# Kernel optimization log

Hardware: AMD Instinct MI355X
Metric: run time of the kernel (lower is better)

## Reference

```python
import jax, jax.numpy as jnp
import numpy as np
from jax import lax

DN = ('NCHW', 'OIHW', 'NCHW')  # torch conv layout
QMIN, QMAX = -128.0, 127.0     # qint8 range


def setup_inputs() -> dict:
    key = jax.random.key(0)
    k1, k2, k3, k4 = jax.random.split(key, 4)
    B, Cin, Cout, H, W, K = 8, 320, 320, 64, 64, 3
    x = jax.random.normal(k1, (B, Cin, H, W), dtype=jnp.float32)
    # int8 weight values stored as int32 (int_repr of per-channel quantized weight)
    weight_int = jax.random.randint(k2, (Cout, Cin, K, K), -128, 128, dtype=jnp.int32)
    weight_scales = jax.random.uniform(k3, (Cout,), jnp.float32, 0.001, 0.01)
    act_scales = jnp.float32(0.04)        # per-tensor activation scale
    act_zero_points = jnp.float32(3.0)    # per-tensor activation zero point
    act_scales_inv = 1.0 / act_scales
    bias = jax.random.normal(k4, (Cout,), dtype=jnp.float32) * 0.1
    # precomputed buffers (from_float): padding>0 path
    weight_sum_by_input_channels = weight_int.astype(jnp.float32).sum(axis=1, keepdims=True)  # [O,1,K,K]
    scale = weight_scales * act_scales  # fused dequant scale per output channel
    return {
        'x': x,
        'weight_int': weight_int,
        'weight_sum_by_input_channels': weight_sum_by_input_channels,
        'scale': scale,
        'act_scales_inv': act_scales_inv,
        'act_zero_points': act_zero_points,
        'bias': bias,
    }


def reference(x, weight_int, weight_sum_by_input_channels, scale,
              act_scales_inv, act_zero_points, bias):
    stride, pad = 1, 1
    # per-tensor activation quantization: x_int = clamp(round(x/s) + zp)
    x_int = jnp.clip(jnp.round(x * act_scales_inv) + act_zero_points, QMIN, QMAX)
    w = weight_int.astype(jnp.float32)
    # integer conv (emulated in f32): conv(x_int, W_int)
    acc = lax.conv_general_dilated(x_int, w, (stride, stride),
                                   [(pad, pad), (pad, pad)], dimension_numbers=DN)
    # zero-point correction: zp * conv(ones, sum_i W_int) (spatially varying near padding)
    ones = jnp.ones_like(x[:, :1])  # [B,1,H,W]
    corr = lax.conv_general_dilated(ones, weight_sum_by_input_channels, (stride, stride),
                                    [(pad, pad), (pad, pad)], dimension_numbers=DN)
    corr = corr * act_zero_points
    # dequant: per-output-channel scale = w_scale * a_scale, plus float bias
    out = scale[None, :, None, None] * (acc - corr) + bias[None, :, None, None]
    return out
```

## Files before the change

kernel.cpp:

```cpp
#include <hip/hip_runtime.h>
#include <hip/hip_bf16.h>


typedef int v4i __attribute__((ext_vector_type(4)));

typedef const unsigned int __attribute__((address_space(1)))* gas_uptr;
typedef unsigned int __attribute__((address_space(3)))* las_uptr;

#define B_   8
#define CIN  320
#define COUT 320
#define H_   64
#define W_   64
#define HW_  4096
#define HP   66
#define WP   66
#define XPAD_BYTES (B_*HP*WP*CIN)
#define W8_BYTES (COUT*9*CIN)

__global__ __launch_bounds__(256) void repack_bias_kernel(const int* __restrict__ wint,
                                                          unsigned char* __restrict__ w8,
                                                          const float* __restrict__ wsum,
                                                          const float* __restrict__ scale,
                                                          const float* __restrict__ bias,
                                                          const float* __restrict__ zp_p,
                                                          float* __restrict__ be) {
    int j = blockIdx.x * 256 + threadIdx.x;
    if (j < COUT) {
        float s = 0.f;
        #pragma unroll
        for (int tp = 0; tp < 9; ++tp) s += wsum[j*9 + tp];
        be[j] = bias[j] - scale[j] * zp_p[0] * s;
    }
    int co  = j / 720;
    int r   = j - co * 720;
    int tap = r / 80;
    int d   = r - tap * 80;
    int ci  = d * 4;
    const int* base = wint + (co * CIN + ci) * 9 + tap;
    unsigned b0 = (unsigned)(base[0]  & 0xFF);
    unsigned b1 = (unsigned)(base[9]  & 0xFF);
    unsigned b2 = (unsigned)(base[18] & 0xFF);
    unsigned b3 = (unsigned)(base[27] & 0xFF);
    unsigned dword = b0 | (b1 << 8) | (b2 << 16) | (b3 << 24);

    int coT   = co >> 4;
    int colc  = co & 15;
    int chunk = ci >> 6;
    int q     = (ci >> 4) & 3;
    int dw    = (ci >> 2) & 3;
    int lane  = q * 16 + colc;
    int idx   = (((coT * 9 + tap) * 5 + chunk) * 64 + lane) * 4 + dw;
    ((unsigned*)w8)[idx] = dword;
}

__global__ __launch_bounds__(256) void quant_pad_kernel(const float* __restrict__ x,
                                                        unsigned char* __restrict__ xpad,
                                                        const float* __restrict__ inv_p,
                                                        const float* __restrict__ zp_p) {
    __shared__ __align__(16) unsigned lds[64 * 81];
    int bid = blockIdx.x;
    int b  = bid / HP;
    int ph = bid - b * HP;
    int t  = threadIdx.x;
    float inv = inv_p[0];
    float zp  = zp_p[0];
    int zpi = (int)rintf(zp);
    unsigned zd = ((unsigned)(zpi & 0xFF)) * 0x01010101u;

    unsigned* rowbase = (unsigned*)(xpad + (size_t)((b * HP + ph) * WP) * CIN);

    if (ph == 0 || ph == HP - 1) {
        for (int j = t; j < WP * CIN / 4; j += 256) rowbase[j] = zd;
        return;
    }
    int h = ph - 1;
    const float* xrow = x + (size_t)b * CIN * H_ * W_ + h * W_;
    int wq = t & 15;
    int cg = t >> 4;
    #pragma unroll
    for (int i = 0; i < 5; ++i) {
        int ci0 = i * 64 + cg * 4;
        float4 f[4];
        #pragma unroll
        for (int jj = 0; jj < 4; ++jj)
            f[jj] = *(const float4*)(xrow + (size_t)(ci0 + jj) * HW_ + wq * 4);
        #pragma unroll
        for (int k = 0; k < 4; ++k) {
            unsigned d = 0;
            #pragma unroll
            for (int jj = 0; jj < 4; ++jj) {
                float v = (&f[jj].x)[k];
                float q = rintf(v * inv) + zp;
                q = fminf(fmaxf(q, -128.0f), 127.0f);
                int qi = (int)q;
                d |= ((unsigned)(qi & 0xFF)) << (8 * jj);
            }
            lds[(wq * 4 + k) * 81 + (ci0 >> 2)] = d;
        }
    }
    __syncthreads();
    if (t < 80)            rowbase[t] = zd;
    else if (t < 160)      rowbase[65 * 80 + (t - 80)] = zd;
    for (int j = t; j < 64 * 80; j += 256) {
        int p = j / 80;
        int d = j - p * 80;
        rowbase[80 + j] = lds[p * 81 + d];
    }
}

#define CHUNK_SLOTS 1584
#define ROUNDS 7
#define BUF_BYTES (ROUNDS * 256 * 16)

#define CHUNK_BODY(c_, LAST_)                                                   \
{                                                                               \
    const int c__ = (c_);                                                       \
    const unsigned char* ab = Al + (c__ & 1) * BUF_BYTES;                       \
          \
    _Pragma("unroll")                                                           \
    for (int k = 0; k < 3; ++k)                                                 \
        _Pragma("unroll")                                                       \
        for (int mi = 0; mi < 4; ++mi)                                          \
            aB[k][mi] = *(const v4i*)(ab + wm * 4224 + aoffs[k][mi]);           \
    _Pragma("unroll")                                                           \
    for (int tp = 0; tp < 9; ++tp) {                                            \
        const int bank = tp % 3;                                                \
        if (!LAST_ && tp == 0) {     \
            unsigned char* dst = Al + ((c__ + 1) & 1) * BUF_BYTES;              \
            int cio = (c__ + 1) * 64;                                           \
            _Pragma("unroll")                                                   \
            for (int r = 0; r < ROUNDS; ++r)                                    \
                __builtin_amdgcn_global_load_lds(                               \
                    (gas_uptr)(const void*)(xpad + srcoff[r] + cio),            \
                    (las_uptr)(dst + r * 4096 + t * 16), 16, 0, 0);             \
        }                                                                       \
                       \
        __builtin_amdgcn_s_setprio(1);                                          \
        _Pragma("unroll")                                                       \
        for (int mi = 0; mi < 4; ++mi)                                          \
            _Pragma("unroll")                                                   \
            for (int ni = 0; ni < 5; ++ni)                                      \
                acc[mi][ni] = __builtin_amdgcn_mfma_i32_16x16x64_i8(            \
                    aB[bank][mi], bB[bank][ni], acc[mi][ni], 0, 0, 0);          \
        __builtin_amdgcn_s_setprio(0);                                          \
           \
           \
        if (tp < 6) {                                                           \
            _Pragma("unroll")                                                   \
            for (int ni = 0; ni < 5; ++ni)                                      \
                bB[bank][ni] = *(const v4i*)(bbase[ni] + ((tp + 3) * 5 + c__) * 1024);\
            int tn  = tp + 3;                                                   \
            int kh2 = tn / 3;                                                   \
            int kw2 = tn - kh2 * 3;                                             \
            _Pragma("unroll")                                                   \
            for (int mi = 0; mi < 4; ++mi)                                      \
                aB[bank][mi] = *(const v4i*)(ab + (wm + kh2) * 4224 + aoffs[kw2][mi]);\
        } else if (!LAST_) {                                                    \
            _Pragma("unroll")                                                   \
            for (int ni = 0; ni < 5; ++ni)                                      \
                bB[bank][ni] = *(const v4i*)(bbase[ni] + ((tp - 6) * 5 + (c__ + 1)) * 1024);\
        }                                                                       \
    }                                                                           \
}

__global__ __launch_bounds__(256, 2) void conv_gemm_kernel(const unsigned char* __restrict__ xpad,
                                                           const unsigned char* __restrict__ w8,
                                                           const float* __restrict__ scale,
                                                           const float* __restrict__ be,
                                                           float* __restrict__ out) {
    __shared__ __align__(16) unsigned char Al[2 * BUF_BYTES];

    int t    = threadIdx.x;
    int lane = t & 63;
    int wave = t >> 6;
    int wm   = wave;
    int m0   = blockIdx.x * 256;
    int n0   = blockIdx.y * 80;
    int b0   = m0 >> 12;
    int h0   = (m0 & 4095) >> 6;

    int srcoff[ROUNDS];
    #pragma unroll
    for (int r = 0; r < ROUNDS; ++r) {
        int slot = r * 256 + t;
        if (slot >= CHUNK_SLOTS) slot = 0;
        int R   = slot / 264;
        int rem = slot - R * 264;
        int C   = rem >> 2;
        int ql  = rem & 3;
        int qs  = ql ^ ((C >> 1) & 3);
        srcoff[r] = ((b0 * HP + h0 + R) * WP + C) * CIN + qs * 16;
    }

    int colc = lane & 15;
    int q    = lane >> 4;

    int aoffs[3][4];
    #pragma unroll
    for (int kw = 0; kw < 3; ++kw)
        #pragma unroll
        for (int mi = 0; mi < 4; ++mi) {
            int C = mi * 16 + colc + kw;
            aoffs[kw][mi] = C * 64 + ((q ^ ((C >> 1) & 3)) * 16);
        }

    const unsigned char* bbase[5];
    int coT0 = n0 >> 4;
    #pragma unroll
    for (int ni = 0; ni < 5; ++ni)
        bbase[ni] = w8 + (size_t)(coT0 + ni) * (45 * 1024) + lane * 16;

    v4i acc[4][5];
    v4i zero = {0, 0, 0, 0};
    #pragma unroll
    for (int mi = 0; mi < 4; ++mi)
        #pragma unroll
        for (int ni = 0; ni < 5; ++ni) acc[mi][ni] = zero;

    v4i bB[3][5], aB[3][4];
    #pragma unroll
    for (int r = 0; r < ROUNDS; ++r)
        __builtin_amdgcn_global_load_lds((gas_uptr)(const void*)(xpad + srcoff[r]),
                                         (las_uptr)(Al + r * 4096 + t * 16), 16, 0, 0);
    #pragma unroll
    for (int k = 0; k < 3; ++k)
        #pragma unroll
        for (int ni = 0; ni < 5; ++ni)
            bB[k][ni] = *(const v4i*)(bbase[ni] + (k * 5) * 1024);

    asm volatile("s_waitcnt vmcnt(15)" ::: "memory");
    __builtin_amdgcn_s_barrier();

    #pragma unroll 1
    for (int c = 0; c < 4; ++c) {
        CHUNK_BODY(c, 0)
        asm volatile("s_waitcnt vmcnt(15)" ::: "memory");
        __builtin_amdgcn_s_barrier();
    }
    CHUNK_BODY(4, 1)

    #pragma unroll
    for (int ni = 0; ni < 5; ++ni) {
        int co = n0 + ni * 16 + colc;
        float s  = scale[co];
        float bz = be[co];
        #pragma unroll
        for (int mi = 0; mi < 4; ++mi) {
            int pix = m0 + wm * 64 + mi * 16 + q * 4;
            int bb2 = pix >> 12;
            int hw  = pix & 4095;
            v4i v = acc[mi][ni];
            float4 o;
            o.x = s * (float)v.x + bz;
            o.y = s * (float)v.y + bz;
            o.z = s * (float)v.z + bz;
            o.w = s * (float)v.w + bz;
            *(float4*)(out + (size_t)(bb2 * COUT + co) * HW_ + hw) = o;
        }
    }
}

extern "C" void kernel_launch(void* const* d_in, const int* in_sizes, int n_in,
                              void* d_out, int out_size, void* d_ws, size_t ws_size,
                              hipStream_t stream) {
    const float* x     = (const float*)d_in[0];
    const int*   wint  = (const int*)d_in[1];
    const float* wsum  = (const float*)d_in[2];
    const float* scale = (const float*)d_in[3];
    const float* inv_p = (const float*)d_in[4];
    const float* zp_p  = (const float*)d_in[5];
    const float* bias  = (const float*)d_in[6];
    float* out = (float*)d_out;

    unsigned char* xpad = (unsigned char*)d_ws;
    unsigned char* w8   = xpad + XPAD_BYTES;
    float*         be   = (float*)(w8 + W8_BYTES);

    repack_bias_kernel<<<(COUT * 720) / 256, 256, 0, stream>>>(wint, w8, wsum, scale, bias, zp_p, be);
    quant_pad_kernel<<<B_ * HP, 256, 0, stream>>>(x, xpad, inv_p, zp_p);

    dim3 grid((B_ * H_ * W_) / 256, COUT / 80);
    conv_gemm_kernel<<<grid, 256, 0, stream>>>(xpad, w8, scale, be, out);
}
```

Baseline: 135.4 us.

## Halve conv GEMM M-tile to two rows and double-buffer operands for higher occupancy

Shrinks each block's pixel tile from four image rows to two: each wave now covers half a row with 2x5 MFMA tiles instead of 4x5. The LDS staging buffer drops from 7 to 5 rounds, and launch bounds rise to 4 blocks per CU. The triple-banked register prefetch becomes a simpler two-slot double buffer that loads the next tap before each MFMA group. The custom vmcnt waits are replaced by plain __syncthreads. The aim is more resident waves and a larger grid to hide latency, at the cost of less weight reuse per block and more halo traffic per output pixel.

```diff
diff --git a/kernel.cpp b/kernel.cpp
--- a/kernel.cpp
+++ b/kernel.cpp
@@ -109,24 +109,25 @@
     }
 }
 
-#define CHUNK_SLOTS 1584
-#define ROUNDS 7
+#define CHUNK_SLOTS 1056
+#define ROUNDS 5
 #define BUF_BYTES (ROUNDS * 256 * 16)
 
 #define CHUNK_BODY(c_, LAST_)                                                   \
 {                                                                               \
     const int c__ = (c_);                                                       \
     const unsigned char* ab = Al + (c__ & 1) * BUF_BYTES;                       \
-          \
+      \
+      \
     _Pragma("unroll")                                                           \
-    for (int k = 0; k < 3; ++k)                                                 \
-        _Pragma("unroll")                                                       \
-        for (int mi = 0; mi < 4; ++mi)                                          \
-            aB[k][mi] = *(const v4i*)(ab + wm * 4224 + aoffs[k][mi]);           \
+    for (int mi = 0; mi < 2; ++mi)                                              \
+        aB[0][mi] = *(const v4i*)(ab + rt * 4224 + aoffs[0][mi]);               \
+    _Pragma("unroll")                                                           \
+    for (int ni = 0; ni < 5; ++ni)                                              \
+        bB[0][ni] = *(const v4i*)(bbase[ni] + c__ * 1024);                      \
     _Pragma("unroll")                                                           \
     for (int tp = 0; tp < 9; ++tp) {                                            \
-        const int bank = tp % 3;                                                \
-        if (!LAST_ && tp == 0) {     \
+        if (!LAST_ && tp == 0) {         \
             unsigned char* dst = Al + ((c__ + 1) & 1) * BUF_BYTES;              \
             int cio = (c__ + 1) * 64;                                           \
             _Pragma("unroll")                                                   \
@@ -135,36 +136,31 @@
                     (gas_uptr)(const void*)(xpad + srcoff[r] + cio),            \
                     (las_uptr)(dst + r * 4096 + t * 16), 16, 0, 0);             \
         }                                                                       \
-                       \
+             \
+             \
+        if (tp < 8) {                                                           \
+            int tn  = tp + 1;                                                   \
+            int kh2 = tn / 3;                                                   \
+            int kw2 = tn - kh2 * 3;                                             \
+            _Pragma("unroll")                                                   \
+            for (int ni = 0; ni < 5; ++ni)                                      \
+                bB[tn & 1][ni] = *(const v4i*)(bbase[ni] + (tn * 5 + c__) * 1024);\
+            _Pragma("unroll")                                                   \
+            for (int mi = 0; mi < 2; ++mi)                                      \
+                aB[tn & 1][mi] = *(const v4i*)(ab + (rt + kh2) * 4224 + aoffs[kw2][mi]);\
+        }                                                                       \
         __builtin_amdgcn_s_setprio(1);                                          \
         _Pragma("unroll")                                                       \
-        for (int mi = 0; mi < 4; ++mi)                                          \
+        for (int mi = 0; mi < 2; ++mi)                                          \
             _Pragma("unroll")                                                   \
             for (int ni = 0; ni < 5; ++ni)                                      \
                 acc[mi][ni] = __builtin_amdgcn_mfma_i32_16x16x64_i8(            \
-                    aB[bank][mi], bB[bank][ni], acc[mi][ni], 0, 0, 0);          \
+                    aB[tp & 1][mi], bB[tp & 1][ni], acc[mi][ni], 0, 0, 0);      \
         __builtin_amdgcn_s_setprio(0);                                          \
-           \
-           \
-        if (tp < 6) {                                                           \
-            _Pragma("unroll")                                                   \
-            for (int ni = 0; ni < 5; ++ni)                                      \
-                bB[bank][ni] = *(const v4i*)(bbase[ni] + ((tp + 3) * 5 + c__) * 1024);\
-            int tn  = tp + 3;                                                   \
-            int kh2 = tn / 3;                                                   \
-            int kw2 = tn - kh2 * 3;                                             \
-            _Pragma("unroll")                                                   \
-            for (int mi = 0; mi < 4; ++mi)                                      \
-                aB[bank][mi] = *(const v4i*)(ab + (wm + kh2) * 4224 + aoffs[kw2][mi]);\
-        } else if (!LAST_) {                                                    \
-            _Pragma("unroll")                                                   \
-            for (int ni = 0; ni < 5; ++ni)                                      \
-                bB[bank][ni] = *(const v4i*)(bbase[ni] + ((tp - 6) * 5 + (c__ + 1)) * 1024);\
-        }                                                                       \
     }                                                                           \
 }
 
-__global__ __launch_bounds__(256, 2) void conv_gemm_kernel(const unsigned char* __restrict__ xpad,
+__global__ __launch_bounds__(256, 4) void conv_gemm_kernel(const unsigned char* __restrict__ xpad,
                                                            const unsigned char* __restrict__ w8,
                                                            const float* __restrict__ scale,
                                                            const float* __restrict__ be,
@@ -174,8 +170,8 @@
     int t    = threadIdx.x;
     int lane = t & 63;
     int wave = t >> 6;
-    int wm   = wave;
-    int m0   = blockIdx.x * 256;
+    int rt   = wave >> 1;
+    int m0   = blockIdx.x * 128;
     int n0   = blockIdx.y * 80;
     int b0   = m0 >> 12;
     int h0   = (m0 & 4095) >> 6;
@@ -196,12 +192,12 @@
     int colc = lane & 15;
     int q    = lane >> 4;
 
-    int aoffs[3][4];
+    int aoffs[3][2];
     #pragma unroll
     for (int kw = 0; kw < 3; ++kw)
         #pragma unroll
-        for (int mi = 0; mi < 4; ++mi) {
-            int C = mi * 16 + colc + kw;
+        for (int mi = 0; mi < 2; ++mi) {
+            int C = (wave & 1) * 32 + mi * 16 + colc + kw;
             aoffs[kw][mi] = C * 64 + ((q ^ ((C >> 1) & 3)) * 16);
         }
 
@@ -211,32 +207,25 @@
     for (int ni = 0; ni < 5; ++ni)
         bbase[ni] = w8 + (size_t)(coT0 + ni) * (45 * 1024) + lane * 16;
 
-    v4i acc[4][5];
+    v4i acc[2][5];
     v4i zero = {0, 0, 0, 0};
     #pragma unroll
-    for (int mi = 0; mi < 4; ++mi)
+    for (int mi = 0; mi < 2; ++mi)
         #pragma unroll
         for (int ni = 0; ni < 5; ++ni) acc[mi][ni] = zero;
 
-    v4i bB[3][5], aB[3][4];
+    v4i bB[2][5], aB[2][2];
+
     #pragma unroll
     for (int r = 0; r < ROUNDS; ++r)
         __builtin_amdgcn_global_load_lds((gas_uptr)(const void*)(xpad + srcoff[r]),
                                          (las_uptr)(Al + r * 4096 + t * 16), 16, 0, 0);
-    #pragma unroll
-    for (int k = 0; k < 3; ++k)
-        #pragma unroll
-        for (int ni = 0; ni < 5; ++ni)
-            bB[k][ni] = *(const v4i*)(bbase[ni] + (k * 5) * 1024);
-
-    asm volatile("s_waitcnt vmcnt(15)" ::: "memory");
-    __builtin_amdgcn_s_barrier();
+    __syncthreads();
 
     #pragma unroll 1
     for (int c = 0; c < 4; ++c) {
         CHUNK_BODY(c, 0)
-        asm volatile("s_waitcnt vmcnt(15)" ::: "memory");
-        __builtin_amdgcn_s_barrier();
+        __syncthreads();
     }
     CHUNK_BODY(4, 1)
 
@@ -246,8 +235,8 @@
         float s  = scale[co];
         float bz = be[co];
         #pragma unroll
-        for (int mi = 0; mi < 4; ++mi) {
-            int pix = m0 + wm * 64 + mi * 16 + q * 4;
+        for (int mi = 0; mi < 2; ++mi) {
+            int pix = m0 + wave * 32 + mi * 16 + q * 4;
             int bb2 = pix >> 12;
             int hw  = pix & 4095;
             v4i v = acc[mi][ni];
@@ -280,6 +269,6 @@
     repack_bias_kernel<<<(COUT * 720) / 256, 256, 0, stream>>>(wint, w8, wsum, scale, bias, zp_p, be);
     quant_pad_kernel<<<B_ * HP, 256, 0, stream>>>(x, xpad, inv_p, zp_p);
 
-    dim3 grid((B_ * H_ * W_) / 256, COUT / 80);
+    dim3 grid((B_ * H_ * W_) / 128, COUT / 80);
     conv_gemm_kernel<<<grid, 256, 0, stream>>>(xpad, w8, scale, be, out);
 }
```

Result: slower. 143.3 us (+5.8%).
